# Kernel optimization log

Measured on AMD Instinct MI355X. Metric: run time of the kernel, lower is better.

The kernel has to match this reference:

```python
import jax, jax.numpy as jnp
import numpy as np

NUM_EMBEDDINGS = 1024
EMBEDDING_DIM = 256
COMMITMENT_COST = 0.25


def setup_inputs() -> dict:
    key = jax.random.key(0)
    k_z, k_e = jax.random.split(key)
    z = jax.random.normal(k_z, (8, EMBEDDING_DIM, 16, 16, 16), dtype=jnp.float32)
    # nn.Embedding weight initialized uniform(-1/K, 1/K)
    codebook = jax.random.uniform(
        k_e, (NUM_EMBEDDINGS, EMBEDDING_DIM), dtype=jnp.float32,
        minval=-1.0 / NUM_EMBEDDINGS, maxval=1.0 / NUM_EMBEDDINGS)
    return {"z": z, "codebook": codebook}


def reference(z, codebook):
    B, D, H, W, L = z.shape
    # (B, D, H, W, L) -> (B, H, W, L, D) -> (N, D)
    z_perm = jnp.transpose(z, (0, 2, 3, 4, 1))          # (B,H,W,L,D)
    z_flat = z_perm.reshape(-1, D)                       # (N,D)
    # squared-distance via expansion: ||z||^2 + ||e||^2 - 2 z.e^T
    distances = ((z_flat ** 2).sum(axis=1, keepdims=True)
                 + (codebook ** 2).sum(axis=1)
                 - 2.0 * z_flat @ codebook.T)            # (N,K)
    indices = jnp.argmin(distances, axis=1)              # (N,)
    quantized = codebook[indices].reshape(B, H, W, L, D)
    idx_out = indices.reshape(B, H, W, L)
    # losses (stop_gradient mirrors .detach())
    e_latent_loss = jnp.mean((jax.lax.stop_gradient(quantized) - z_perm) ** 2)
    q_latent_loss = jnp.mean((quantized - jax.lax.stop_gradient(z_perm)) ** 2)
    vq_loss = q_latent_loss + COMMITMENT_COST * e_latent_loss
    # straight-through estimator
    quant_st = z_perm + jax.lax.stop_gradient(quantized - z_perm)
    quant_out = jnp.transpose(quant_st, (0, 4, 1, 2, 3))  # (B,D,H,W,L)
    return quant_out, idx_out, vq_loss
```

## Files before the change

### kernel.cpp

```cpp
#include <hip/hip_runtime.h>


#define K_CODES 1024
#define DIM 256
#define N_TOK 32768
#define SPATIAL 4096
#define TOK_BLK 64
#define NBLK (N_TOK / TOK_BLK)
#define CAP 28
#define MARGIN 1e-3f

typedef __attribute__((ext_vector_type(8))) short short8;
typedef __attribute__((ext_vector_type(4))) float float4v;

#define WS_LOSS 0
#define WS_CNT 8
#define WS_E2 16
#define WS_EB 2048

#define O_IDX (8 * DIM * SPATIAL)
#define O_LOSS (O_IDX + N_TOK)

__device__ __forceinline__ short f2bf(float v) {
  unsigned u = __float_as_uint(v);
  u = (u + 0x7fffu + ((u >> 16) & 1u)) >> 16;
  return (short)u;
}

__global__ __launch_bounds__(256) void prep_kernel(const float* __restrict__ e,
                                                   float* __restrict__ ws) {
  __shared__ float sq[DIM];
  __shared__ __align__(16) short sbf[DIM];
  __shared__ float chv[16];
  int k = blockIdx.x, d = threadIdx.x;
  float v = e[k * DIM + d];
  sbf[d] = f2bf(v);
  sq[d] = __fmul_rn(v, v);
  __syncthreads();
  if (d < 32) {
    int f = d >> 2, q = d & 3;
    int stage = k >> 6, ct = (k >> 4) & 3, nn = k & 15;
    short8 chunk = *(const short8*)(sbf + f * 32 + q * 8);
    int off8 = ((stage * 4 + ct) * 8 + f) * 64 + q * 16 + nn;
    ((short8*)(ws + WS_EB))[off8] = chunk;
  }
  if (d < 16) {
    int blkb = d >> 3, j = d & 7;
    const float* x = sq + blkb * 128;
    float c = x[j];
#pragma unroll
    for (int i = 1; i < 16; i++) c = __fadd_rn(c, x[i * 8 + j]);
    chv[d] = c;
  }
  __syncthreads();
  if (d == 0) {
    float a0 = __fadd_rn(__fadd_rn(chv[0], chv[1]), __fadd_rn(chv[2], chv[3]));
    float a1 = __fadd_rn(__fadd_rn(chv[4], chv[5]), __fadd_rn(chv[6], chv[7]));
    float resA = __fadd_rn(a0, a1);
    float b0 = __fadd_rn(__fadd_rn(chv[8], chv[9]), __fadd_rn(chv[10], chv[11]));
    float b1 = __fadd_rn(__fadd_rn(chv[12], chv[13]), __fadd_rn(chv[14], chv[15]));
    float resB = __fadd_rn(b0, b1);
    ws[WS_E2 + k] = __fadd_rn(resA, resB);
    if (k == 0) {
      ws[WS_LOSS] = 0.f;
      ((unsigned*)ws)[WS_CNT] = 0u;
    }
  }
}

__global__ __launch_bounds__(512, 4) void main_kernel(const float* __restrict__ z,
                                                      const float* __restrict__ e,
                                                      float* __restrict__ ws,
                                                      float* __restrict__ out) {
  __shared__ __align__(16) short Bst[64 * 256];
  __shared__ unsigned short cand[TOK_BLK][CAP];
  __shared__ float cands[TOK_BLK][CAP];
  __shared__ float aminv[2][TOK_BLK];
  __shared__ int cnt[TOK_BLK];
  __shared__ float Szp[2][TOK_BLK];
  __shared__ int mini_sh[TOK_BLK];
  __shared__ float red[8];

  int tid = threadIdx.x, w = tid >> 6, lane = tid & 63;
  int quad = lane >> 4, nn = lane & 15;
  int g = w & 3, kh = w >> 2;
  int n0 = blockIdx.x * TOK_BLK;
  int b = n0 >> 12, s0 = n0 & 4095;
  const float* zb = z + (size_t)b * DIM * SPATIAL + s0;
  const float* Se = ws + WS_E2;
  const uint4* eBg = (const uint4*)(ws + WS_EB);
  if (tid < TOK_BLK) cnt[tid] = 0;

  {
    const float* zp = zb + g * 16 + nn;
    float r0, r1;
    {
      int j0 = quad * 2;
      float v0 = zp[(size_t)(kh * 128 + j0) * SPATIAL];
      float v1 = zp[(size_t)(kh * 128 + j0 + 1) * SPATIAL];
      r0 = __fmul_rn(v0, v0);
      r1 = __fmul_rn(v1, v1);
      for (int i = 1; i < 16; i++) {
        v0 = zp[(size_t)(kh * 128 + i * 8 + j0) * SPATIAL];
        v1 = zp[(size_t)(kh * 128 + i * 8 + j0 + 1) * SPATIAL];
        r0 = __fadd_rn(r0, __fmul_rn(v0, v0));
        r1 = __fadd_rn(r1, __fmul_rn(v1, v1));
      }
    }
    float p = __fadd_rn(r0, r1);
    float s1 = __fadd_rn(p, __shfl_xor(p, 16));
    float s2 = __fadd_rn(s1, __shfl_xor(s1, 32));
    if (quad == 0) Szp[kh][g * 16 + nn] = s2;
  }

  int tokA = g * 16 + nn;
  short8 A[8];
#pragma unroll
  for (int f = 0; f < 8; f++) {
    short8 a;
#pragma unroll
    for (int j = 0; j < 8; j++) {
      int d = f * 32 + quad * 8 + j;
      a[j] = f2bf(zb[(size_t)d * SPATIAL + tokA]);
    }
    A[f] = a;
  }

  float thr[4] = {3.4e38f, 3.4e38f, 3.4e38f, 3.4e38f};
  for (int stage = 0; stage < 16; stage++) {
    __syncthreads();
#pragma unroll
    for (int i = 0; i < 4; i++)
      ((uint4*)Bst)[i * 512 + tid] = eBg[(size_t)stage * 2048 + i * 512 + tid];
    __syncthreads();

    int ct0 = kh * 2, ct1 = kh * 2 + 1;
    int kbase0 = stage * 64 + ct0 * 16;
    int kbase1 = stage * 64 + ct1 * 16;
    float4v C0 = {0.f, 0.f, 0.f, 0.f};
    float4v C1 = {0.f, 0.f, 0.f, 0.f};
    const short8* Bp0 = (const short8*)Bst + ct0 * 8 * 64;
    const short8* Bp1 = (const short8*)Bst + ct1 * 8 * 64;
#pragma unroll
    for (int f = 0; f < 8; f++) {
      short8 B0 = Bp0[f * 64 + lane];
      short8 B1 = Bp1[f * 64 + lane];
      C0 = __builtin_amdgcn_mfma_f32_16x16x32_bf16(A[f], B0, C0, 0, 0, 0);
      C1 = __builtin_amdgcn_mfma_f32_16x16x32_bf16(A[f], B1, C1, 0, 0, 0);
    }
    float SeK0 = Se[kbase0 + nn];
    float SeK1 = Se[kbase1 + nn];
    float s0[4], s1[4], m0[4], m1[4];
#pragma unroll
    for (int r = 0; r < 4; r++) {
      s0[r] = fmaf(-2.f, C0[r], SeK0);
      s1[r] = fmaf(-2.f, C1[r], SeK1);
      m0[r] = s0[r];
      m1[r] = s1[r];
    }
#pragma unroll
    for (int dlt = 1; dlt <= 8; dlt <<= 1) {
#pragma unroll
      for (int r = 0; r < 4; r++) {
        m0[r] = fminf(m0[r], __shfl_xor(m0[r], dlt, 16));
        m1[r] = fminf(m1[r], __shfl_xor(m1[r], dlt, 16));
      }
    }
    bool pr[4];
#pragma unroll
    for (int r = 0; r < 4; r++) {
      thr[r] = fminf(thr[r], m0[r]);
      pr[r] = s0[r] < thr[r] + MARGIN;
    }
    if (__ballot(pr[0] | pr[1] | pr[2] | pr[3])) {
#pragma unroll
      for (int r = 0; r < 4; r++) {
        unsigned long long bl = __ballot(pr[r]);
        unsigned grp = (unsigned)((bl >> (quad * 16)) & 0xffffULL);
        if (grp) {
          int tb = g * 16 + quad * 4 + r;
          int base = 0;
          if (nn == 0) base = atomicAdd(&cnt[tb], __popc(grp));
          base = __shfl(base, quad * 16);
          if (pr[r]) {
            int pos = base + __popc(grp & ((1u << nn) - 1u));
            if (pos < CAP) {
              cand[tb][pos] = (unsigned short)(kbase0 + nn);
              cands[tb][pos] = s0[r];
            }
          }
        }
      }
    }
#pragma unroll
    for (int r = 0; r < 4; r++) {
      thr[r] = fminf(thr[r], m1[r]);
      pr[r] = s1[r] < thr[r] + MARGIN;
    }
    if (__ballot(pr[0] | pr[1] | pr[2] | pr[3])) {
#pragma unroll
      for (int r = 0; r < 4; r++) {
        unsigned long long bl = __ballot(pr[r]);
        unsigned grp = (unsigned)((bl >> (quad * 16)) & 0xffffULL);
        if (grp) {
          int tb = g * 16 + quad * 4 + r;
          int base = 0;
          if (nn == 0) base = atomicAdd(&cnt[tb], __popc(grp));
          base = __shfl(base, quad * 16);
          if (pr[r]) {
            int pos = base + __popc(grp & ((1u << nn) - 1u));
            if (pos < CAP) {
              cand[tb][pos] = (unsigned short)(kbase1 + nn);
              cands[tb][pos] = s1[r];
            }
          }
        }
      }
    }
  }
#pragma unroll
  for (int r = 0; r < 4; r++)
    if (nn == 0) aminv[kh][g * 16 + quad * 4 + r] = thr[r];
  __syncthreads();

  int tl = lane >> 3, oct = lane & 7;
  int tb = w * 8 + tl;
  int cc = cnt[tb];
  int cl = cc < CAP ? cc : CAP;
  float bestD = 3.4e38f;
  int bestk = 0x7fffffff;
  float SznT = __fadd_rn(Szp[0][tb], Szp[1][tb]);
  {
    const float* zp = zb + tb;
    float amin = fminf(aminv[0][tb], aminv[1][tb]);
    for (int c = oct; c < cl; c += 8) {
      if (cands[tb][c] >= amin + MARGIN) continue;
      int k = cand[tb][c];
      const float* er = e + (size_t)k * DIM;
      float acc = 0.f;
#pragma unroll 4
      for (int dd = 0; dd < DIM; dd += 4) {
        float4 e4 = *(const float4*)(er + dd);
        acc = fmaf(zp[(size_t)(dd + 0) * SPATIAL], e4.x, acc);
        acc = fmaf(zp[(size_t)(dd + 1) * SPATIAL], e4.y, acc);
        acc = fmaf(zp[(size_t)(dd + 2) * SPATIAL], e4.z, acc);
        acc = fmaf(zp[(size_t)(dd + 3) * SPATIAL], e4.w, acc);
      }
      float D = __fsub_rn(__fadd_rn(SznT, Se[k]), __fmul_rn(2.f, acc));
      if (D < bestD || (D == bestD && k < bestk)) { bestD = D; bestk = k; }
    }
  }
#pragma unroll
  for (int off = 4; off >= 1; off >>= 1) {
    float oD = __shfl_down(bestD, off, 8);
    int ok = __shfl_down(bestk, off, 8);
    if (oD < bestD || (oD == bestD && ok < bestk)) { bestD = oD; bestk = ok; }
  }
  if (oct == 0 && cc <= CAP) {
    mini_sh[tb] = bestk;
    out[O_IDX + n0 + tb] = (float)bestk;
  }
  for (int t = 0; t < 8; t++) {
    int tb2 = w * 8 + t;
    if (cnt[tb2] > CAP) {
      const float* zq = zb + tb2;
      float Szn = __fadd_rn(Szp[0][tb2], Szp[1][tb2]);
      float bD = 3.4e38f;
      int bk = 0x7fffffff;
      for (int k = lane; k < K_CODES; k += 64) {
        const float* er = e + (size_t)k * DIM;
        float acc = 0.f;
#pragma unroll 4
        for (int dd = 0; dd < DIM; dd += 4) {
          float4 e4 = *(const float4*)(er + dd);
          acc = fmaf(zq[(size_t)(dd + 0) * SPATIAL], e4.x, acc);
          acc = fmaf(zq[(size_t)(dd + 1) * SPATIAL], e4.y, acc);
          acc = fmaf(zq[(size_t)(dd + 2) * SPATIAL], e4.z, acc);
          acc = fmaf(zq[(size_t)(dd + 3) * SPATIAL], e4.w, acc);
        }
        float D = __fsub_rn(__fadd_rn(Szn, Se[k]), __fmul_rn(2.f, acc));
        if (D < bD || (D == bD && k < bk)) { bD = D; bk = k; }
      }
#pragma unroll
      for (int m = 1; m < 64; m <<= 1) {
        float oD = __shfl_xor(bD, m);
        int ok = __shfl_xor(bk, m);
        if (oD < bD || (oD == bD && ok < bk)) { bD = oD; bk = ok; }
      }
      if (lane == 0) {
        mini_sh[tb2] = bk;
        out[O_IDX + n0 + tb2] = (float)bk;
      }
    }
  }
  __syncthreads();

  int mten = mini_sh[lane];
  const float* erow = e + (size_t)mten * DIM;
  float* op = out + (size_t)b * DIM * SPATIAL + s0;
  float sumsq = 0.f;
#pragma unroll 2
  for (int i4 = 0; i4 < 32; i4 += 4) {
    int d = w * 32 + i4;
    float4 v4 = *(const float4*)(erow + d);
#pragma unroll
    for (int m = 0; m < 4; m++) {
      float v = (m == 0) ? v4.x : (m == 1) ? v4.y : (m == 2) ? v4.z : v4.w;
      float zv = zb[(size_t)(d + m) * SPATIAL + lane];
      float df = __fsub_rn(v, zv);
      sumsq = fmaf(df, df, sumsq);
      op[(size_t)(d + m) * SPATIAL + lane] = v;
    }
  }
#pragma unroll
  for (int o = 32; o > 0; o >>= 1) sumsq += __shfl_down(sumsq, o, 64);
  if (lane == 0) red[w] = sumsq;
  __syncthreads();
  if (tid == 0) {
    float rs = ((red[0] + red[1]) + (red[2] + red[3])) +
               ((red[4] + red[5]) + (red[6] + red[7]));
    atomicAdd(ws + WS_LOSS, rs);
    __threadfence();
    unsigned t = atomicAdd((unsigned*)ws + WS_CNT, 1u);
    if (t == NBLK - 1) {
      float total = atomicAdd(ws + WS_LOSS, 0.f);
      out[O_LOSS] = 1.25f * total / 8388608.f;
    }
  }
}

extern "C" void kernel_launch(void* const* d_in, const int* in_sizes, int n_in,
                              void* d_out, int out_size, void* d_ws, size_t ws_size,
                              hipStream_t stream) {
  const float* z = (const float*)d_in[0];
  const float* e = (const float*)d_in[1];
  float* ws = (float*)d_ws;
  float* out = (float*)d_out;

  prep_kernel<<<K_CODES, 256, 0, stream>>>(e, ws);
  main_kernel<<<NBLK, 512, 0, stream>>>(z, e, ws, out);
}
```

Measured before the change: 202.1 us.

## Split fused VQ kernel into filter, recheck and epilogue kernels

```diff
diff --git a/kernel.cpp b/kernel.cpp
--- a/kernel.cpp
+++ b/kernel.cpp
@@ -17,6 +17,9 @@
 #define WS_CNT 8
 #define WS_E2 16
 #define WS_EB 2048
+#define WS_SZ 133120
+#define WS_CAND 165888
+#define WS_CCNT 624640
 
 #define O_IDX (8 * DIM * SPATIAL)
 #define O_LOSS (O_IDX + N_TOK)
@@ -68,18 +71,12 @@
   }
 }
 
-__global__ __launch_bounds__(512, 4) void main_kernel(const float* __restrict__ z,
-                                                      const float* __restrict__ e,
-                                                      float* __restrict__ ws,
-                                                      float* __restrict__ out) {
+__global__ __launch_bounds__(512, 4) void filter_kernel(const float* __restrict__ z,
+                                                        float* __restrict__ ws) {
   __shared__ __align__(16) short Bst[64 * 256];
   __shared__ unsigned short cand[TOK_BLK][CAP];
-  __shared__ float cands[TOK_BLK][CAP];
-  __shared__ float aminv[2][TOK_BLK];
   __shared__ int cnt[TOK_BLK];
   __shared__ float Szp[2][TOK_BLK];
-  __shared__ int mini_sh[TOK_BLK];
-  __shared__ float red[8];
 
   int tid = threadIdx.x, w = tid >> 6, lane = tid & 63;
   int quad = lane >> 4, nn = lane & 15;
@@ -150,13 +147,13 @@
     }
     float SeK0 = Se[kbase0 + nn];
     float SeK1 = Se[kbase1 + nn];
-    float s0[4], s1[4], m0[4], m1[4];
+    float s0v[4], s1v[4], m0[4], m1[4];
 #pragma unroll
     for (int r = 0; r < 4; r++) {
-      s0[r] = fmaf(-2.f, C0[r], SeK0);
-      s1[r] = fmaf(-2.f, C1[r], SeK1);
-      m0[r] = s0[r];
-      m1[r] = s1[r];
+      s0v[r] = fmaf(-2.f, C0[r], SeK0);
+      s1v[r] = fmaf(-2.f, C1[r], SeK1);
+      m0[r] = s0v[r];
+      m1[r] = s1v[r];
     }
 #pragma unroll
     for (int dlt = 1; dlt <= 8; dlt <<= 1) {
@@ -170,7 +167,7 @@
 #pragma unroll
     for (int r = 0; r < 4; r++) {
       thr[r] = fminf(thr[r], m0[r]);
-      pr[r] = s0[r] < thr[r] + MARGIN;
+      pr[r] = s0v[r] < thr[r] + MARGIN;
     }
     if (__ballot(pr[0] | pr[1] | pr[2] | pr[3])) {
 #pragma unroll
@@ -184,10 +181,7 @@
           base = __shfl(base, quad * 16);
           if (pr[r]) {
             int pos = base + __popc(grp & ((1u << nn) - 1u));
-            if (pos < CAP) {
-              cand[tb][pos] = (unsigned short)(kbase0 + nn);
-              cands[tb][pos] = s0[r];
-            }
+            if (pos < CAP) cand[tb][pos] = (unsigned short)(kbase0 + nn);
           }
         }
       }
@@ -195,7 +189,7 @@
 #pragma unroll
     for (int r = 0; r < 4; r++) {
       thr[r] = fminf(thr[r], m1[r]);
-      pr[r] = s1[r] < thr[r] + MARGIN;
+      pr[r] = s1v[r] < thr[r] + MARGIN;
     }
     if (__ballot(pr[0] | pr[1] | pr[2] | pr[3])) {
 #pragma unroll
@@ -209,33 +203,51 @@
           base = __shfl(base, quad * 16);
           if (pr[r]) {
             int pos = base + __popc(grp & ((1u << nn) - 1u));
-            if (pos < CAP) {
-              cand[tb][pos] = (unsigned short)(kbase1 + nn);
-              cands[tb][pos] = s1[r];
-            }
+            if (pos < CAP) cand[tb][pos] = (unsigned short)(kbase1 + nn);
           }
         }
       }
     }
   }
-#pragma unroll
-  for (int r = 0; r < 4; r++)
-    if (nn == 0) aminv[kh][g * 16 + quad * 4 + r] = thr[r];
   __syncthreads();
 
+  {
+    int t = tid >> 3, j = tid & 7;
+    int cv = cnt[t];
+    if (j == 0) ((int*)ws)[WS_CCNT + n0 + t] = cv;
+    if (j == 1)
+      ws[WS_SZ + n0 + t] = __fadd_rn(Szp[0][t], Szp[1][t]);
+    int cl = cv < CAP ? cv : CAP;
+    unsigned short* cg = (unsigned short*)(ws + WS_CAND) + (size_t)(n0 + t) * CAP;
+    for (int c = j; c < cl; c += 8) cg[c] = cand[t][c];
+  }
+}
+
+__global__ __launch_bounds__(256, 8) void recheck_kernel(const float* __restrict__ z,
+                                                         const float* __restrict__ e,
+                                                         float* __restrict__ ws,
+                                                         float* __restrict__ out) {
+  int tid = threadIdx.x, w = tid >> 6, lane = tid & 63;
   int tl = lane >> 3, oct = lane & 7;
+  int n0 = blockIdx.x * 32;
+  int b = n0 >> 12, s0 = n0 & 4095;
+  const float* zb = z + (size_t)b * DIM * SPATIAL + s0;
+  const float* Se = ws + WS_E2;
+  const unsigned short* candg = (const unsigned short*)(ws + WS_CAND);
+  const int* cntg = (const int*)ws + WS_CCNT;
+
   int tb = w * 8 + tl;
-  int cc = cnt[tb];
+  int tok = n0 + tb;
+  int cc = cntg[tok];
   int cl = cc < CAP ? cc : CAP;
+  float Szn = ws[WS_SZ + tok];
   float bestD = 3.4e38f;
   int bestk = 0x7fffffff;
-  float SznT = __fadd_rn(Szp[0][tb], Szp[1][tb]);
   {
     const float* zp = zb + tb;
-    float amin = fminf(aminv[0][tb], aminv[1][tb]);
+    const unsigned short* cg = candg + (size_t)tok * CAP;
     for (int c = oct; c < cl; c += 8) {
-      if (cands[tb][c] >= amin + MARGIN) continue;
-      int k = cand[tb][c];
+      int k = cg[c];
       const float* er = e + (size_t)k * DIM;
       float acc = 0.f;
 #pragma unroll 4
@@ -246,7 +258,7 @@
         acc = fmaf(zp[(size_t)(dd + 2) * SPATIAL], e4.z, acc);
         acc = fmaf(zp[(size_t)(dd + 3) * SPATIAL], e4.w, acc);
       }
-      float D = __fsub_rn(__fadd_rn(SznT, Se[k]), __fmul_rn(2.f, acc));
+      float D = __fsub_rn(__fadd_rn(Szn, Se[k]), __fmul_rn(2.f, acc));
       if (D < bestD || (D == bestD && k < bestk)) { bestD = D; bestk = k; }
     }
   }
@@ -256,15 +268,12 @@
     int ok = __shfl_down(bestk, off, 8);
     if (oD < bestD || (oD == bestD && ok < bestk)) { bestD = oD; bestk = ok; }
   }
-  if (oct == 0 && cc <= CAP) {
-    mini_sh[tb] = bestk;
-    out[O_IDX + n0 + tb] = (float)bestk;
-  }
+  if (oct == 0 && cc <= CAP) out[O_IDX + tok] = (float)bestk;
   for (int t = 0; t < 8; t++) {
     int tb2 = w * 8 + t;
-    if (cnt[tb2] > CAP) {
+    if (cntg[n0 + tb2] > CAP) {
       const float* zq = zb + tb2;
-      float Szn = __fadd_rn(Szp[0][tb2], Szp[1][tb2]);
+      float Sz2 = ws[WS_SZ + n0 + tb2];
       float bD = 3.4e38f;
       int bk = 0x7fffffff;
       for (int k = lane; k < K_CODES; k += 64) {
@@ -278,7 +287,7 @@
           acc = fmaf(zq[(size_t)(dd + 2) * SPATIAL], e4.z, acc);
           acc = fmaf(zq[(size_t)(dd + 3) * SPATIAL], e4.w, acc);
         }
-        float D = __fsub_rn(__fadd_rn(Szn, Se[k]), __fmul_rn(2.f, acc));
+        float D = __fsub_rn(__fadd_rn(Sz2, Se[k]), __fmul_rn(2.f, acc));
         if (D < bD || (D == bD && k < bk)) { bD = D; bk = k; }
       }
 #pragma unroll
@@ -287,21 +296,27 @@
         int ok = __shfl_xor(bk, m);
         if (oD < bD || (oD == bD && ok < bk)) { bD = oD; bk = ok; }
       }
-      if (lane == 0) {
-        mini_sh[tb2] = bk;
-        out[O_IDX + n0 + tb2] = (float)bk;
-      }
-    }
-  }
-  __syncthreads();
-
-  int mten = mini_sh[lane];
+      if (lane == 0) out[O_IDX + n0 + tb2] = (float)bk;
+    }
+  }
+}
+
+__global__ __launch_bounds__(256, 4) void epilogue_kernel(const float* __restrict__ z,
+                                                          const float* __restrict__ e,
+                                                          float* __restrict__ ws,
+                                                          float* __restrict__ out) {
+  __shared__ float red[4];
+  int tid = threadIdx.x, w = tid >> 6, lane = tid & 63;
+  int n0 = blockIdx.x * TOK_BLK;
+  int b = n0 >> 12, s0 = n0 & 4095;
+  const float* zb = z + (size_t)b * DIM * SPATIAL + s0;
+  int mten = (int)out[O_IDX + n0 + lane];
   const float* erow = e + (size_t)mten * DIM;
   float* op = out + (size_t)b * DIM * SPATIAL + s0;
   float sumsq = 0.f;
-#pragma unroll 2
-  for (int i4 = 0; i4 < 32; i4 += 4) {
-    int d = w * 32 + i4;
+#pragma unroll 4
+  for (int i4 = 0; i4 < 64; i4 += 4) {
+    int d = w * 64 + i4;
     float4 v4 = *(const float4*)(erow + d);
 #pragma unroll
     for (int m = 0; m < 4; m++) {
@@ -317,9 +332,7 @@
   if (lane == 0) red[w] = sumsq;
   __syncthreads();
   if (tid == 0) {
-    float rs = ((red[0] + red[1]) + (red[2] + red[3])) +
-               ((red[4] + red[5]) + (red[6] + red[7]));
-    atomicAdd(ws + WS_LOSS, rs);
+    atomicAdd(ws + WS_LOSS, red[0] + red[1] + red[2] + red[3]);
     __threadfence();
     unsigned t = atomicAdd((unsigned*)ws + WS_CNT, 1u);
     if (t == NBLK - 1) {
@@ -338,5 +351,7 @@
   float* out = (float*)d_out;
 
   prep_kernel<<<K_CODES, 256, 0, stream>>>(e, ws);
-  main_kernel<<<NBLK, 512, 0, stream>>>(z, e, ws, out);
-}
+  filter_kernel<<<NBLK, 512, 0, stream>>>(z, ws);
+  recheck_kernel<<<N_TOK / 32, 256, 0, stream>>>(z, e, ws, out);
+  epilogue_kernel<<<NBLK, 256, 0, stream>>>(z, e, ws, out);
+}
```

Measured after the change: 234.9 us. 1.16x slower.
